# Optimization experiments

Hardware: AMD Instinct MI355X
Metric: run time of the kernel (lower is better)

Reference implementation:

```python
import jax, jax.numpy as jnp
import numpy as np

B, T, F, U, M, OUT = 2048, 16, 512, 512, 8, 3
DELTA_T = 0.04
EPS = 1e-07


def setup_inputs() -> dict:
    key = jax.random.key(0)
    ks = jax.random.split(key, 6)
    s_in = 1.0 / np.sqrt(F + U)
    s_u = 1.0 / np.sqrt(U)
    return {
        "x": jax.random.normal(ks[0], (B, T, F), dtype=jnp.float32),
        "W_r": jax.random.normal(ks[1], (F + U, U * M), dtype=jnp.float32) * s_in,
        "b_r": jnp.zeros((U * M,), dtype=jnp.float32),
        "W_q": jax.random.normal(ks[2], (F + U, U), dtype=jnp.float32) * s_in,
        "b_q": jnp.zeros((U,), dtype=jnp.float32),
        "W_s": jax.random.normal(ks[3], (F + U, U * M), dtype=jnp.float32) * s_in,
        "b_s": jnp.zeros((U * M,), dtype=jnp.float32),
        "W_o": jax.random.normal(ks[4], (U, OUT), dtype=jnp.float32) * s_u,
        "b_o": jnp.zeros((OUT,), dtype=jnp.float32),
    }


def _ln_tau_table():
    # tau_i = 10^(i/2)  =>  ln tau_i = i * 0.5 * ln(10)
    return (jnp.arange(M, dtype=jnp.float32) * (0.5 * np.log(10.0)))


def reference(x, W_r, b_r, W_q, b_q, W_s, b_s, W_o, b_o):
    ln_tau = _ln_tau_table()                       # (M,)
    decay = jnp.exp(-DELTA_T / (jnp.exp(ln_tau) + EPS))  # (M,)

    def step(h_hat, x_t):
        # h_hat: (B, U, M), x_t: (B, F)
        h = h_hat.sum(axis=2)                       # (B, U)
        fi = jnp.concatenate([x_t, h], axis=1)      # (B, F+U)
        ln_r = (fi @ W_r + b_r).reshape(-1, U, M)
        r = jax.nn.softmax(-jnp.square(ln_r - ln_tau), axis=2)
        ctx = jnp.sum(r * h_hat, axis=2)            # (B, U)
        q = jnp.tanh(jnp.concatenate([x_t, ctx], axis=1) @ W_q + b_q)[:, :, None]
        ln_s = (fi @ W_s + b_s).reshape(-1, U, M)
        s = jax.nn.softmax(-jnp.square(ln_s - ln_tau), axis=2)
        h_hat_next = ((1.0 - s) * h_hat + s * q) * decay
        hidden = h_hat_next.sum(axis=2)             # (B, U)
        return h_hat_next, hidden

    h0 = jnp.zeros((x.shape[0], U, M), dtype=x.dtype)
    xs = jnp.swapaxes(x, 0, 1)                      # (T, B, F)
    _, hs = jax.lax.scan(step, h0, xs)              # hs: (T, B, U)
    hs = jnp.swapaxes(hs, 0, 1)                     # (B, T, U)
    out = hs @ W_o + b_o                            # (B, T, OUT)
    return out
```

## Files before the change

kernel.cpp:

```cpp
#include <hip/hip_runtime.h>
#include <math.h>

#define B_ 2048
#define T_ 16
#define F_ 512
#define U_ 512
#define M_ 8

typedef _Float16 half8 __attribute__((ext_vector_type(8)));
typedef float f32x4 __attribute__((ext_vector_type(4)));

__device__ __forceinline__ void load_lds16(const _Float16* gsrc, _Float16* lds) {
    __builtin_amdgcn_global_load_lds(
        (const __attribute__((address_space(1))) void*)gsrc,
        (__attribute__((address_space(3))) void*)lds, 16, 0, 0);
}

#define BAR() __builtin_amdgcn_s_barrier()
#define LGKM0() asm volatile("s_waitcnt lgkmcnt(0)" ::: "memory")
#define VMW(n) asm volatile("s_waitcnt vmcnt(" #n ")" ::: "memory")
#define MFMA16(a, b, c) __builtin_amdgcn_mfma_f32_16x16x32_f16(a, b, c, 0, 0, 0)

struct Decay8 { float d[8]; };

__global__ __launch_bounds__(256) void cast_x_kernel(const float* __restrict__ in,
                                                     _Float16* __restrict__ out) {
    long i = (long)blockIdx.x * 256 + threadIdx.x;
    const f32x4* p = (const f32x4*)in;
    f32x4 a = p[i * 2], b = p[i * 2 + 1];
    half8 v;
    v[0] = (_Float16)a[0]; v[1] = (_Float16)a[1]; v[2] = (_Float16)a[2]; v[3] = (_Float16)a[3];
    v[4] = (_Float16)b[0]; v[5] = (_Float16)b[1]; v[6] = (_Float16)b[2]; v[7] = (_Float16)b[3];
    ((half8*)out)[i] = v;
}

__global__ __launch_bounds__(256) void transpose_cast_kernel(const float* __restrict__ W,
                                                             _Float16* __restrict__ Wt,
                                                             int K, int N) {
    __shared__ float tile[32][33];
    int n0 = blockIdx.x * 32, k0 = blockIdx.y * 32;
    int tx = threadIdx.x, ty = threadIdx.y;
    #pragma unroll
    for (int i = 0; i < 32; i += 8)
        tile[ty + i][tx] = W[(long)(k0 + ty + i) * N + n0 + tx];
    __syncthreads();
    #pragma unroll
    for (int i = 0; i < 32; i += 8)
        Wt[(long)(n0 + ty + i) * K + k0 + tx] = (_Float16)tile[tx][ty + i];
}

__global__ __launch_bounds__(256) void transpose_cast_perm_kernel(const float* __restrict__ W,
                                                                  _Float16* __restrict__ Wt,
                                                                  int rowbase) {
    const int K = 1024, N = 4096;
    __shared__ float tile[32][33];
    int n0 = blockIdx.x * 32, k0 = blockIdx.y * 32;
    int tx = threadIdx.x, ty = threadIdx.y;
    #pragma unroll
    for (int i = 0; i < 32; i += 8)
        tile[ty + i][tx] = W[(long)(k0 + ty + i) * N + n0 + tx];
    __syncthreads();
    #pragma unroll
    for (int i = 0; i < 32; i += 8) {
        int nl = n0 + ty + i;
        int u = nl >> 3, m = nl & 7;
        int nn = ((u >> 4) << 7) + (m << 4) + (u & 15);
        Wt[(long)(rowbase + nn) * K + k0 + tx] = (_Float16)tile[tx][ty + i];
    }
}

__global__ __launch_bounds__(512, 2) void gemm1_fused_kernel(
    const _Float16* __restrict__ A0, long lda0,
    const _Float16* __restrict__ A1, long lda1,
    const _Float16* __restrict__ Wt,
    const float* __restrict__ b_r, const float* __restrict__ b_s,
    const _Float16* __restrict__ h_hat,
    _Float16* __restrict__ ctx,
    _Float16* __restrict__ s_buf) {
    constexpr int NT = 16;
    const float LT = 1.1512925464970228f;
    __shared__ __align__(16) _Float16 As[2][256 * 64];
    __shared__ __align__(16) _Float16 Bs[2][256 * 64];
    const int tid = threadIdx.x;
    const int lane = tid & 63;
    const int wave = tid >> 6;
    const int wm = wave >> 1, wn = wave & 1;
    const int l15 = lane & 15, lhi = lane >> 4, swz = lane & 7;
    const int g0 = (lhi ^ swz) * 8;
    const int g1 = ((lhi + 4) ^ swz) * 8;
    const int srow = tid >> 3;
    const int sg = (tid & 7) ^ (srow & 7);
    const int ldsdst = wave * 64 * 8;
    const long m0 = (long)blockIdx.y * 256;
    const long n0 = (long)blockIdx.x * 256;

#define STAGE_A(kt_, buf_, r_) do {                                             \
        int kt__ = (kt_);                                                       \
        const _Float16* s_; long lda_; int kofs_;                               \
        if (kt__ < 8) { s_ = A0; lda_ = lda0; kofs_ = kt__ * 64; }              \
        else          { s_ = A1; lda_ = lda1; kofs_ = kt__ * 64 - 512; }        \
        load_lds16(s_ + (m0 + (r_) * 64 + srow) * lda_ + kofs_ + sg * 8,        \
                   &As[buf_][(r_) * 4096 + ldsdst]);                            \
    } while (0)
#define STAGE_B(kt_, buf_, r_)                                                  \
        load_lds16(Wt + (n0 + (r_) * 64 + srow) * 1024 + (kt_) * 64 + sg * 8,   \
                   &Bs[buf_][(r_) * 4096 + ldsdst])

    f32x4 acc[4][8] = {};

    #pragma unroll
    for (int r = 0; r < 4; ++r) STAGE_A(0, 0, r);
    #pragma unroll
    for (int r = 0; r < 4; ++r) STAGE_B(0, 0, r);
    #pragma unroll
    for (int r = 0; r < 4; ++r) STAGE_A(1, 1, r);
    STAGE_B(1, 1, 0); STAGE_B(1, 1, 2);
    VMW(6);
    BAR();

    #pragma unroll 1
    for (int t = 0; t < NT; ++t) {
        const int cur = t & 1, nxt = cur ^ 1;
        const _Float16* Ac = &As[cur][0];
        const _Float16* Bc = &Bs[cur][0];
        half8 af[4][2], bfa[2][2], bfb[2][2];

        #pragma unroll
        for (int i = 0; i < 4; ++i) {
            const _Float16* p = Ac + (wm * 64 + i * 16 + l15) * 64;
            af[i][0] = *(const half8*)(p + g0);
            af[i][1] = *(const half8*)(p + g1);
        }
        #pragma unroll
        for (int j = 0; j < 2; ++j) {
            const _Float16* p = Bc + (wn * 128 + j * 16 + l15) * 64;
            bfa[j][0] = *(const half8*)(p + g0);
            bfa[j][1] = *(const half8*)(p + g1);
        }
        if (t + 1 < NT) { STAGE_B(t + 1, nxt, 1); STAGE_B(t + 1, nxt, 3); }
        BAR(); LGKM0();
        __builtin_amdgcn_s_setprio(1);
        #pragma unroll
        for (int i = 0; i < 4; ++i)
            #pragma unroll
            for (int j = 0; j < 2; ++j) {
                acc[i][j] = MFMA16(af[i][0], bfa[j][0], acc[i][j]);
                acc[i][j] = MFMA16(af[i][1], bfa[j][1], acc[i][j]);
            }
        __builtin_amdgcn_s_setprio(0);
        BAR();

        #pragma unroll
        for (int j = 0; j < 2; ++j) {
            const _Float16* p = Bc + (wn * 128 + (2 + j) * 16 + l15) * 64;
            bfb[j][0] = *(const half8*)(p + g0);
            bfb[j][1] = *(const half8*)(p + g1);
        }
        if (t + 2 < NT) { STAGE_A(t + 2, cur, 0); STAGE_A(t + 2, cur, 1); }
        BAR(); LGKM0();
        __builtin_amdgcn_s_setprio(1);
        #pragma unroll
        for (int i = 0; i < 4; ++i)
            #pragma unroll
            for (int j = 0; j < 2; ++j) {
                acc[i][2 + j] = MFMA16(af[i][0], bfb[j][0], acc[i][2 + j]);
                acc[i][2 + j] = MFMA16(af[i][1], bfb[j][1], acc[i][2 + j]);
            }
        __builtin_amdgcn_s_setprio(0);
        BAR();

        #pragma unroll
        for (int j = 0; j < 2; ++j) {
            const _Float16* p = Bc + (wn * 128 + (4 + j) * 16 + l15) * 64;
            bfa[j][0] = *(const half8*)(p + g0);
            bfa[j][1] = *(const half8*)(p + g1);
        }
        if (t + 2 < NT) { STAGE_A(t + 2, cur, 2); STAGE_A(t + 2, cur, 3); }
        BAR(); LGKM0();
        __builtin_amdgcn_s_setprio(1);
        #pragma unroll
        for (int i = 0; i < 4; ++i)
            #pragma unroll
            for (int j = 0; j < 2; ++j) {
                acc[i][4 + j] = MFMA16(af[i][0], bfa[j][0], acc[i][4 + j]);
                acc[i][4 + j] = MFMA16(af[i][1], bfa[j][1], acc[i][4 + j]);
            }
        __builtin_amdgcn_s_setprio(0);
        BAR();

        #pragma unroll
        for (int j = 0; j < 2; ++j) {
            const _Float16* p = Bc + (wn * 128 + (6 + j) * 16 + l15) * 64;
            bfb[j][0] = *(const half8*)(p + g0);
            bfb[j][1] = *(const half8*)(p + g1);
        }
        if (t + 2 < NT) { STAGE_B(t + 2, cur, 0); STAGE_B(t + 2, cur, 2); }
        LGKM0();
        __builtin_amdgcn_s_setprio(1);
        #pragma unroll
        for (int i = 0; i < 4; ++i)
            #pragma unroll
            for (int j = 0; j < 2; ++j) {
                acc[i][6 + j] = MFMA16(af[i][0], bfb[j][0], acc[i][6 + j]);
                acc[i][6 + j] = MFMA16(af[i][1], bfb[j][1], acc[i][6 + j]);
            }
        __builtin_amdgcn_s_setprio(0);
        if (t + 2 < NT)      { VMW(6); }
        else if (t + 1 < NT) { VMW(0); }
        BAR();
    }

    const int r4 = lhi * 4;
    const int panel = (int)(n0 >> 7) + wn;
    const bool is_r = panel < 32;
    const int u = (is_r ? panel : panel - 32) * 16 + l15;
    const float* bias = is_r ? b_r : b_s;
    f32x4 bl0 = *(const f32x4*)(bias + u * 8);
    f32x4 bl1 = *(const f32x4*)(bias + u * 8 + 4);

    #pragma unroll
    for (int i = 0; i < 4; ++i) {
        #pragma unroll
        for (int r = 0; r < 4; ++r) {
            long m = m0 + wm * 64 + i * 16 + r4 + r;
            float z[8]; float zmax = -1e30f;
            #pragma unroll
            for (int j = 0; j < 8; ++j) {
                float v = acc[i][j][r] + (j < 4 ? bl0[j] : bl1[j - 4]);
                float d = v - (float)j * LT;
                z[j] = -d * d;
                zmax = fmaxf(zmax, z[j]);
            }
            float e[8]; float se = 0.f;
            #pragma unroll
            for (int j = 0; j < 8; ++j) { e[j] = __expf(z[j] - zmax); se += e[j]; }
            float inv = 1.f / se;
            if (is_r) {
                half8 hh = *(const half8*)(h_hat + m * 4096 + u * 8);
                float c = 0.f;
                #pragma unroll
                for (int j = 0; j < 8; ++j) c += e[j] * (float)hh[j];
                ctx[m * 512 + u] = (_Float16)(c * inv);
            } else {
                half8 sv;
                #pragma unroll
                for (int j = 0; j < 8; ++j) sv[j] = (_Float16)(e[j] * inv);
                *(half8*)(s_buf + m * 4096 + u * 8) = sv;
            }
        }
    }
#undef STAGE_A
#undef STAGE_B
}

__global__ __launch_bounds__(512) void gemm2_fused_kernel(
    const _Float16* __restrict__ A0, long lda0,
    const _Float16* __restrict__ A1, long lda1,
    const _Float16* __restrict__ Wt,
    const float* __restrict__ bias,
    const _Float16* __restrict__ s_buf,
    _Float16* __restrict__ h_hat,
    _Float16* __restrict__ hs_t,
    Decay8 dec) {
    constexpr int NT = 16;
    __shared__ __align__(16) _Float16 As[2][64 * 64];
    __shared__ __align__(16) _Float16 Bs[2][64 * 64];
    const int tid = threadIdx.x;
    const int lane = tid & 63;
    const int wave = tid >> 6;
    const int wm = wave >> 1, wn = wave & 1;
    const int l15 = lane & 15, lhi = lane >> 4, swz = lane & 7;
    const int g0 = (lhi ^ swz) * 8;
    const int g1 = ((lhi + 4) ^ swz) * 8;
    const int srow = tid >> 3;
    const int sg = (tid & 7) ^ (srow & 7);
    const long m0 = (long)blockIdx.y * 64;
    const long n0 = (long)blockIdx.x * 64;

#define STAGE2(kt_, buf_) do {                                                  \
        int kt__ = (kt_);                                                       \
        const _Float16* s_; long lda_; int kofs_;                               \
        if (kt__ < 8) { s_ = A0; lda_ = lda0; kofs_ = kt__ * 64; }              \
        else          { s_ = A1; lda_ = lda1; kofs_ = kt__ * 64 - 512; }        \
        load_lds16(s_ + (m0 + srow) * lda_ + kofs_ + sg * 8,                    \
                   &As[buf_][wave * 512]);                                      \
        load_lds16(Wt + (n0 + srow) * 1024 + kt__ * 64 + sg * 8,                \
                   &Bs[buf_][wave * 512]);                                      \
    } while (0)

    f32x4 acc[2] = {};

    STAGE2(0, 0);
    #pragma unroll 1
    for (int kt = 0; kt < NT; ++kt) {
        const int cur = kt & 1;
        if (kt + 1 < NT) { STAGE2(kt + 1, cur ^ 1); VMW(2); }
        else             { VMW(0); }
        BAR();
        const _Float16* Ac = &As[cur][0];
        const _Float16* Bc = &Bs[cur][0];
        half8 af[2], bf[2][2];
        {
            const _Float16* p = Ac + (wm * 16 + l15) * 64;
            af[0] = *(const half8*)(p + g0);
            af[1] = *(const half8*)(p + g1);
        }
        #pragma unroll
        for (int j = 0; j < 2; ++j) {
            const _Float16* p = Bc + (wn * 32 + j * 16 + l15) * 64;
            bf[j][0] = *(const half8*)(p + g0);
            bf[j][1] = *(const half8*)(p + g1);
        }
        LGKM0();
        #pragma unroll
        for (int j = 0; j < 2; ++j) {
            acc[j] = MFMA16(af[0], bf[j][0], acc[j]);
            acc[j] = MFMA16(af[1], bf[j][1], acc[j]);
        }
        BAR();
    }
#undef STAGE2

    const int r4 = lhi * 4;
    #pragma unroll
    for (int j = 0; j < 2; ++j) {
        #pragma unroll
        for (int r = 0; r < 4; ++r) {
            long b = m0 + wm * 16 + r4 + r;
            long u = n0 + wn * 32 + j * 16 + l15;
            float q = tanhf(acc[j][r] + bias[u]);
            half8 s8 = *(const half8*)(s_buf + b * 4096 + u * 8);
            half8 h8 = *(const half8*)(h_hat + b * 4096 + u * 8);
            half8 hn;
            float hval = 0.f;
            #pragma unroll
            for (int m = 0; m < 8; ++m) {
                float sm = (float)s8[m];
                float x = ((1.f - sm) * (float)h8[m] + sm * q) * dec.d[m];
                hn[m] = (_Float16)x;
                hval += x;
            }
            *(half8*)(h_hat + b * 4096 + u * 8) = hn;
            hs_t[b * 512 + u] = (_Float16)hval;
        }
    }
}

__global__ __launch_bounds__(64) void out_proj_kernel(const _Float16* __restrict__ hs,
                                                      const float* __restrict__ W_o,
                                                      const float* __restrict__ b_o,
                                                      float* __restrict__ out) {
    const int bt = blockIdx.x;
    const int t = bt >> 11, b = bt & 2047;
    const int lane = threadIdx.x;
    half8 v = *(const half8*)(hs + ((long)t * 2048 + b) * 512 + lane * 8);
    float p0 = 0.f, p1 = 0.f, p2 = 0.f;
    #pragma unroll
    for (int m = 0; m < 8; ++m) {
        float hv = (float)v[m];
        int u = lane * 8 + m;
        p0 += hv * W_o[u * 3 + 0];
        p1 += hv * W_o[u * 3 + 1];
        p2 += hv * W_o[u * 3 + 2];
    }
    #pragma unroll
    for (int s = 32; s > 0; s >>= 1) {
        p0 += __shfl_down(p0, s);
        p1 += __shfl_down(p1, s);
        p2 += __shfl_down(p2, s);
    }
    if (lane == 0) {
        long o = ((long)b * T_ + t) * 3;
        out[o + 0] = p0 + b_o[0];
        out[o + 1] = p1 + b_o[1];
        out[o + 2] = p2 + b_o[2];
    }
}

extern "C" void kernel_launch(void* const* d_in, const int* in_sizes, int n_in,
                              void* d_out, int out_size, void* d_ws, size_t ws_size,
                              hipStream_t stream) {
    const float* x   = (const float*)d_in[0];
    const float* W_r = (const float*)d_in[1];
    const float* b_r = (const float*)d_in[2];
    const float* W_q = (const float*)d_in[3];
    const float* b_q = (const float*)d_in[4];
    const float* W_s = (const float*)d_in[5];
    const float* b_s = (const float*)d_in[6];
    const float* W_o = (const float*)d_in[7];
    const float* b_o = (const float*)d_in[8];
    float* out = (float*)d_out;

    char* ws = (char*)d_ws;
    size_t off = 0;
    _Float16* x_h   = (_Float16*)(ws + off); off += (size_t)B_ * T_ * F_ * 2;
    _Float16* Wrs_t = (_Float16*)(ws + off); off += (size_t)8192 * 1024 * 2;
    _Float16* Wq_t  = (_Float16*)(ws + off); off += (size_t)512 * 1024 * 2;
    _Float16* s_buf = (_Float16*)(ws + off); off += (size_t)B_ * 4096 * 2;
    _Float16* h_hat = (_Float16*)(ws + off); off += (size_t)B_ * 4096 * 2;
    _Float16* ctx_h = (_Float16*)(ws + off); off += (size_t)B_ * U_ * 2;
    _Float16* hs    = (_Float16*)(ws + off); off += (size_t)T_ * B_ * U_ * 2;
    _Float16* zbuf  = (_Float16*)(ws + off); off += (size_t)B_ * U_ * 2;
    if (ws_size < off) return;

    hipMemsetAsync(h_hat, 0, (size_t)B_ * 4096 * 2, stream);
    hipMemsetAsync(zbuf, 0, (size_t)B_ * U_ * 2, stream);

    cast_x_kernel<<<dim3((B_ * T_ * F_) / (256 * 8)), 256, 0, stream>>>(x, x_h);
    transpose_cast_perm_kernel<<<dim3(4096 / 32, 1024 / 32), dim3(32, 8), 0, stream>>>(W_r, Wrs_t, 0);
    transpose_cast_perm_kernel<<<dim3(4096 / 32, 1024 / 32), dim3(32, 8), 0, stream>>>(W_s, Wrs_t, 4096);
    transpose_cast_kernel<<<dim3(512 / 32, 1024 / 32), dim3(32, 8), 0, stream>>>(W_q, Wq_t, 1024, 512);

    Decay8 dec;
    for (int m = 0; m < 8; ++m) {
        float lt = (float)m * 1.1512925464970228f;
        dec.d[m] = expf(-0.04f / (expf(lt) + 1e-7f));
    }

    for (int t = 0; t < T_; ++t) {
        const _Float16* hprev = (t == 0) ? zbuf : hs + (size_t)(t - 1) * B_ * U_;
        gemm1_fused_kernel<<<dim3(8192 / 256, B_ / 256), 512, 0, stream>>>(
            x_h + (long)t * F_, (long)T_ * F_, hprev, U_, Wrs_t,
            b_r, b_s, h_hat, ctx_h, s_buf);
        gemm2_fused_kernel<<<dim3(512 / 64, B_ / 64), 512, 0, stream>>>(
            x_h + (long)t * F_, (long)T_ * F_, ctx_h, U_, Wq_t,
            b_q, s_buf, h_hat, hs + (size_t)t * B_ * U_, dec);
    }
    out_proj_kernel<<<dim3(B_ * T_), 64, 0, stream>>>(hs, W_o, b_o, out);
    (void)in_sizes; (void)n_in; (void)out_size;
}
```

Measured before the change: 1.006 ms.

## Use 16-wave gemm1 blocks with 64x64 warp tiles and split softmax across lanes

```diff
diff --git a/kernel.cpp b/kernel.cpp
--- a/kernel.cpp
+++ b/kernel.cpp
@@ -8,6 +8,7 @@
 #define M_ 8
 
 typedef _Float16 half8 __attribute__((ext_vector_type(8)));
+typedef _Float16 half4 __attribute__((ext_vector_type(4)));
 typedef float f32x4 __attribute__((ext_vector_type(4)));
 
 __device__ __forceinline__ void load_lds16(const _Float16* gsrc, _Float16* lds) {
@@ -64,12 +65,12 @@
     for (int i = 0; i < 32; i += 8) {
         int nl = n0 + ty + i;
         int u = nl >> 3, m = nl & 7;
-        int nn = ((u >> 4) << 7) + (m << 4) + (u & 15);
+        int nn = ((u >> 3) << 6) + ((m & 3) << 4) + ((m >> 2) << 3) + (u & 7);
         Wt[(long)(rowbase + nn) * K + k0 + tx] = (_Float16)tile[tx][ty + i];
     }
 }
 
-__global__ __launch_bounds__(512, 2) void gemm1_fused_kernel(
+__global__ __launch_bounds__(1024) void gemm1_fused_kernel(
     const _Float16* __restrict__ A0, long lda0,
     const _Float16* __restrict__ A1, long lda1,
     const _Float16* __restrict__ Wt,
@@ -84,173 +85,171 @@
     const int tid = threadIdx.x;
     const int lane = tid & 63;
     const int wave = tid >> 6;
-    const int wm = wave >> 1, wn = wave & 1;
+    const int wm = wave >> 2, wn = wave & 3;
     const int l15 = lane & 15, lhi = lane >> 4, swz = lane & 7;
     const int g0 = (lhi ^ swz) * 8;
     const int g1 = ((lhi + 4) ^ swz) * 8;
     const int srow = tid >> 3;
     const int sg = (tid & 7) ^ (srow & 7);
-    const int ldsdst = wave * 64 * 8;
+    const int bb = (wave >> 2) * 64 + (wave & 3) * 8;
     const long m0 = (long)blockIdx.y * 256;
     const long n0 = (long)blockIdx.x * 256;
 
-#define STAGE_A(kt_, buf_, r_) do {                                             \
+#define STAGE_A2(kt_, buf_, r_) do {                                            \
         int kt__ = (kt_);                                                       \
         const _Float16* s_; long lda_; int kofs_;                               \
         if (kt__ < 8) { s_ = A0; lda_ = lda0; kofs_ = kt__ * 64; }              \
         else          { s_ = A1; lda_ = lda1; kofs_ = kt__ * 64 - 512; }        \
-        load_lds16(s_ + (m0 + (r_) * 64 + srow) * lda_ + kofs_ + sg * 8,        \
-                   &As[buf_][(r_) * 4096 + ldsdst]);                            \
+        load_lds16(s_ + (m0 + (r_) * 128 + srow) * lda_ + kofs_ + sg * 8,       \
+                   &As[buf_][(r_) * 8192 + wave * 512]);                        \
     } while (0)
-#define STAGE_B(kt_, buf_, r_)                                                  \
-        load_lds16(Wt + (n0 + (r_) * 64 + srow) * 1024 + (kt_) * 64 + sg * 8,   \
-                   &Bs[buf_][(r_) * 4096 + ldsdst])
-
-    f32x4 acc[4][8] = {};
-
-    #pragma unroll
-    for (int r = 0; r < 4; ++r) STAGE_A(0, 0, r);
-    #pragma unroll
-    for (int r = 0; r < 4; ++r) STAGE_B(0, 0, r);
-    #pragma unroll
-    for (int r = 0; r < 4; ++r) STAGE_A(1, 1, r);
-    STAGE_B(1, 1, 0); STAGE_B(1, 1, 2);
-    VMW(6);
+#define STAGE_B2(kt_, buf_, r_)                                                 \
+        load_lds16(Wt + (n0 + (r_) * 128 + srow) * 1024 + (kt_) * 64 + sg * 8,  \
+                   &Bs[buf_][(r_) * 8192 + wave * 512])
+#define STAGE_B_CLS(kt_, buf_, c_)                                              \
+        load_lds16(Wt + (n0 + bb + (c_) * 32 + ((tid >> 3) & 7)) * 1024 +       \
+                       (kt_) * 64 + sg * 8,                                     \
+                   &Bs[buf_][(bb + (c_) * 32) * 64])
+
+    f32x4 acc[4][4] = {};
+
+    STAGE_A2(0, 0, 0); STAGE_A2(0, 0, 1);
+    STAGE_B2(0, 0, 0); STAGE_B2(0, 0, 1);
+    STAGE_A2(1, 1, 0); STAGE_A2(1, 1, 1);
+    STAGE_B2(1, 1, 0); STAGE_B2(1, 1, 1);
+    VMW(4);
     BAR();
 
     #pragma unroll 1
     for (int t = 0; t < NT; ++t) {
-        const int cur = t & 1, nxt = cur ^ 1;
+        const int cur = t & 1;
         const _Float16* Ac = &As[cur][0];
         const _Float16* Bc = &Bs[cur][0];
-        half8 af[4][2], bfa[2][2], bfb[2][2];
-
-        #pragma unroll
-        for (int i = 0; i < 4; ++i) {
+        half8 af01[2][2], af23[2][2], bf01[2][2], bf23[2][2];
+
+        #pragma unroll
+        for (int i = 0; i < 2; ++i) {
             const _Float16* p = Ac + (wm * 64 + i * 16 + l15) * 64;
-            af[i][0] = *(const half8*)(p + g0);
-            af[i][1] = *(const half8*)(p + g1);
+            af01[i][0] = *(const half8*)(p + g0);
+            af01[i][1] = *(const half8*)(p + g1);
         }
         #pragma unroll
         for (int j = 0; j < 2; ++j) {
-            const _Float16* p = Bc + (wn * 128 + j * 16 + l15) * 64;
-            bfa[j][0] = *(const half8*)(p + g0);
-            bfa[j][1] = *(const half8*)(p + g1);
-        }
-        if (t + 1 < NT) { STAGE_B(t + 1, nxt, 1); STAGE_B(t + 1, nxt, 3); }
+            const _Float16* p = Bc + (wn * 64 + j * 16 + l15) * 64;
+            bf01[j][0] = *(const half8*)(p + g0);
+            bf01[j][1] = *(const half8*)(p + g1);
+        }
         BAR(); LGKM0();
         __builtin_amdgcn_s_setprio(1);
         #pragma unroll
-        for (int i = 0; i < 4; ++i)
+        for (int i = 0; i < 2; ++i)
             #pragma unroll
             for (int j = 0; j < 2; ++j) {
-                acc[i][j] = MFMA16(af[i][0], bfa[j][0], acc[i][j]);
-                acc[i][j] = MFMA16(af[i][1], bfa[j][1], acc[i][j]);
+                acc[i][j] = MFMA16(af01[i][0], bf01[j][0], acc[i][j]);
+                acc[i][j] = MFMA16(af01[i][1], bf01[j][1], acc[i][j]);
             }
         __builtin_amdgcn_s_setprio(0);
         BAR();
 
         #pragma unroll
-        for (int j = 0; j < 2; ++j) {
-            const _Float16* p = Bc + (wn * 128 + (2 + j) * 16 + l15) * 64;
-            bfb[j][0] = *(const half8*)(p + g0);
-            bfb[j][1] = *(const half8*)(p + g1);
-        }
-        if (t + 2 < NT) { STAGE_A(t + 2, cur, 0); STAGE_A(t + 2, cur, 1); }
+        for (int i = 0; i < 2; ++i) {
+            const _Float16* p = Ac + (wm * 64 + (2 + i) * 16 + l15) * 64;
+            af23[i][0] = *(const half8*)(p + g0);
+            af23[i][1] = *(const half8*)(p + g1);
+        }
+        if (t + 2 < NT) { STAGE_B_CLS(t + 2, cur, 0); }
         BAR(); LGKM0();
         __builtin_amdgcn_s_setprio(1);
         #pragma unroll
-        for (int i = 0; i < 4; ++i)
+        for (int i = 0; i < 2; ++i)
             #pragma unroll
             for (int j = 0; j < 2; ++j) {
-                acc[i][2 + j] = MFMA16(af[i][0], bfb[j][0], acc[i][2 + j]);
-                acc[i][2 + j] = MFMA16(af[i][1], bfb[j][1], acc[i][2 + j]);
+                acc[2 + i][j] = MFMA16(af23[i][0], bf01[j][0], acc[2 + i][j]);
+                acc[2 + i][j] = MFMA16(af23[i][1], bf01[j][1], acc[2 + i][j]);
             }
         __builtin_amdgcn_s_setprio(0);
         BAR();
 
         #pragma unroll
         for (int j = 0; j < 2; ++j) {
-            const _Float16* p = Bc + (wn * 128 + (4 + j) * 16 + l15) * 64;
-            bfa[j][0] = *(const half8*)(p + g0);
-            bfa[j][1] = *(const half8*)(p + g1);
-        }
-        if (t + 2 < NT) { STAGE_A(t + 2, cur, 2); STAGE_A(t + 2, cur, 3); }
+            const _Float16* p = Bc + (wn * 64 + (2 + j) * 16 + l15) * 64;
+            bf23[j][0] = *(const half8*)(p + g0);
+            bf23[j][1] = *(const half8*)(p + g1);
+        }
+        if (t + 2 < NT) { STAGE_A2(t + 2, cur, 0); STAGE_A2(t + 2, cur, 1); }
         BAR(); LGKM0();
         __builtin_amdgcn_s_setprio(1);
         #pragma unroll
-        for (int i = 0; i < 4; ++i)
+        for (int i = 0; i < 2; ++i)
             #pragma unroll
             for (int j = 0; j < 2; ++j) {
-                acc[i][4 + j] = MFMA16(af[i][0], bfa[j][0], acc[i][4 + j]);
-                acc[i][4 + j] = MFMA16(af[i][1], bfa[j][1], acc[i][4 + j]);
+                acc[2 + i][2 + j] = MFMA16(af23[i][0], bf23[j][0], acc[2 + i][2 + j]);
+                acc[2 + i][2 + j] = MFMA16(af23[i][1], bf23[j][1], acc[2 + i][2 + j]);
             }
         __builtin_amdgcn_s_setprio(0);
         BAR();
 
-        #pragma unroll
-        for (int j = 0; j < 2; ++j) {
-            const _Float16* p = Bc + (wn * 128 + (6 + j) * 16 + l15) * 64;
-            bfb[j][0] = *(const half8*)(p + g0);
-            bfb[j][1] = *(const half8*)(p + g1);
-        }
-        if (t + 2 < NT) { STAGE_B(t + 2, cur, 0); STAGE_B(t + 2, cur, 2); }
-        LGKM0();
+        if (t + 2 < NT) { STAGE_B_CLS(t + 2, cur, 1); }
+        BAR();
         __builtin_amdgcn_s_setprio(1);
         #pragma unroll
-        for (int i = 0; i < 4; ++i)
+        for (int i = 0; i < 2; ++i)
             #pragma unroll
             for (int j = 0; j < 2; ++j) {
-                acc[i][6 + j] = MFMA16(af[i][0], bfb[j][0], acc[i][6 + j]);
-                acc[i][6 + j] = MFMA16(af[i][1], bfb[j][1], acc[i][6 + j]);
+                acc[i][2 + j] = MFMA16(af01[i][0], bf23[j][0], acc[i][2 + j]);
+                acc[i][2 + j] = MFMA16(af01[i][1], bf23[j][1], acc[i][2 + j]);
             }
         __builtin_amdgcn_s_setprio(0);
-        if (t + 2 < NT)      { VMW(6); }
+        if (t + 2 < NT)      { VMW(4); }
         else if (t + 1 < NT) { VMW(0); }
         BAR();
     }
 
     const int r4 = lhi * 4;
-    const int panel = (int)(n0 >> 7) + wn;
-    const bool is_r = panel < 32;
-    const int u = (is_r ? panel : panel - 32) * 16 + l15;
+    const int q = (int)(n0 >> 6) + wn;
+    const bool is_r = q < 64;
+    const int ul = l15 & 7, h = l15 >> 3;
+    const int u = (is_r ? q : q - 64) * 8 + ul;
     const float* bias = is_r ? b_r : b_s;
-    f32x4 bl0 = *(const f32x4*)(bias + u * 8);
-    f32x4 bl1 = *(const f32x4*)(bias + u * 8 + 4);
+    f32x4 bl = *(const f32x4*)(bias + u * 8 + h * 4);
 
     #pragma unroll
     for (int i = 0; i < 4; ++i) {
         #pragma unroll
         for (int r = 0; r < 4; ++r) {
             long m = m0 + wm * 64 + i * 16 + r4 + r;
-            float z[8]; float zmax = -1e30f;
-            #pragma unroll
-            for (int j = 0; j < 8; ++j) {
-                float v = acc[i][j][r] + (j < 4 ? bl0[j] : bl1[j - 4]);
-                float d = v - (float)j * LT;
+            float z[4]; float zm = -1e30f;
+            #pragma unroll
+            for (int j = 0; j < 4; ++j) {
+                float v = acc[i][j][r] + bl[j];
+                float d = v - (float)(4 * h + j) * LT;
                 z[j] = -d * d;
-                zmax = fmaxf(zmax, z[j]);
-            }
-            float e[8]; float se = 0.f;
-            #pragma unroll
-            for (int j = 0; j < 8; ++j) { e[j] = __expf(z[j] - zmax); se += e[j]; }
+                zm = fmaxf(zm, z[j]);
+            }
+            zm = fmaxf(zm, __shfl_xor(zm, 8));
+            float e[4]; float se = 0.f;
+            #pragma unroll
+            for (int j = 0; j < 4; ++j) { e[j] = __expf(z[j] - zm); se += e[j]; }
+            se += __shfl_xor(se, 8);
             float inv = 1.f / se;
             if (is_r) {
-                half8 hh = *(const half8*)(h_hat + m * 4096 + u * 8);
+                half4 hh = *(const half4*)(h_hat + m * 4096 + u * 8 + h * 4);
                 float c = 0.f;
                 #pragma unroll
-                for (int j = 0; j < 8; ++j) c += e[j] * (float)hh[j];
-                ctx[m * 512 + u] = (_Float16)(c * inv);
+                for (int j = 0; j < 4; ++j) c += e[j] * (float)hh[j];
+                c += __shfl_xor(c, 8);
+                if (h == 0) ctx[m * 512 + u] = (_Float16)(c * inv);
             } else {
-                half8 sv;
+                half4 sv;
                 #pragma unroll
-                for (int j = 0; j < 8; ++j) sv[j] = (_Float16)(e[j] * inv);
-                *(half8*)(s_buf + m * 4096 + u * 8) = sv;
-            }
-        }
-    }
-#undef STAGE_A
-#undef STAGE_B
+                for (int j = 0; j < 4; ++j) sv[j] = (_Float16)(e[j] * inv);
+                *(half4*)(s_buf + m * 4096 + u * 8 + h * 4) = sv;
+            }
+        }
+    }
+#undef STAGE_A2
+#undef STAGE_B2
+#undef STAGE_B_CLS
 }
 
 __global__ __launch_bounds__(512) void gemm2_fused_kernel(
@@ -322,12 +321,13 @@
 #undef STAGE2
 
     const int r4 = lhi * 4;
+    const int c16 = lane & 15;
     #pragma unroll
     for (int j = 0; j < 2; ++j) {
         #pragma unroll
         for (int r = 0; r < 4; ++r) {
             long b = m0 + wm * 16 + r4 + r;
-            long u = n0 + wn * 32 + j * 16 + l15;
+            long u = n0 + wn * 32 + j * 16 + c16;
             float q = tanhf(acc[j][r] + bias[u]);
             half8 s8 = *(const half8*)(s_buf + b * 4096 + u * 8);
             half8 h8 = *(const half8*)(h_hat + b * 4096 + u * 8);
@@ -419,7 +419,7 @@
 
     for (int t = 0; t < T_; ++t) {
         const _Float16* hprev = (t == 0) ? zbuf : hs + (size_t)(t - 1) * B_ * U_;
-        gemm1_fused_kernel<<<dim3(8192 / 256, B_ / 256), 512, 0, stream>>>(
+        gemm1_fused_kernel<<<dim3(8192 / 256, B_ / 256), 1024, 0, stream>>>(
             x_h + (long)t * F_, (long)T_ * F_, hprev, U_, Wrs_t,
             b_r, b_s, h_hat, ctx_h, s_buf);
         gemm2_fused_kernel<<<dim3(512 / 64, B_ / 64), 512, 0, stream>>>(
```

Measured after the change: 1.315 ms. 1.31x slower.
